# Kernel optimization log

Measured on AMD Instinct MI355X. Metric: run time of the kernel, lower is better.

## Reference

```python
import jax, jax.numpy as jnp
import numpy as np

B, C, H, W = 8, 512, 48, 48
DK = C // 8            # query/key dim
L = max(H, W)          # rel_pos_length == H == W
R = 2 * L - 1          # num relative shifts
N = H * W
EPS = 1e-5


def setup_inputs() -> dict:
    key = jax.random.key(0)
    ks = jax.random.split(key, 20)
    d = {
        "x": jax.random.normal(ks[0], (B, C, H, W), jnp.float32),
        "Wq": jax.random.normal(ks[1], (DK, C), jnp.float32) * 0.02,
        "bq": jnp.zeros((DK,), jnp.float32),
        "q_scale": jnp.ones((DK,), jnp.float32),
        "q_bias": jnp.zeros((DK,), jnp.float32),
        "Wk": jax.random.normal(ks[2], (DK, C), jnp.float32) * 0.02,
        "bk": jnp.zeros((DK,), jnp.float32),
        "k_scale": jnp.ones((DK,), jnp.float32),
        "k_bias": jnp.zeros((DK,), jnp.float32),
        "Wv": jax.random.normal(ks[3], (C, C), jnp.float32) * 0.02,
        "bv": jnp.zeros((C,), jnp.float32),
        "v_scale": jnp.ones((C,), jnp.float32),
        "v_bias": jnp.zeros((C,), jnp.float32),
        "rel_rows": jax.random.normal(ks[4], (R, DK), jnp.float32),
        "rel_columns": jax.random.normal(ks[5], (R, DK), jnp.float32),
        "bnr_scale": jnp.ones((C,), jnp.float32),
        "bnr_bias": jnp.zeros((C,), jnp.float32),
        "bnc_scale": jnp.ones((C,), jnp.float32),
        "bnc_bias": jnp.zeros((C,), jnp.float32),
        # gamma is a learned scalar (init 0 in torch; nonzero here so output != x)
        "gamma": jax.random.normal(ks[6], (1,), jnp.float32) * 0.1,
    }
    return d


def _bn(y, scale, bias):
    # train-mode BatchNorm2d: batch stats over (B,H,W), biased variance
    m = jnp.mean(y, axis=(0, 2, 3))
    v = jnp.mean((y - m[None, :, None, None]) ** 2, axis=(0, 2, 3))
    yn = (y - m[None, :, None, None]) * jax.lax.rsqrt(v + EPS)[None, :, None, None]
    return yn * scale[None, :, None, None] + bias[None, :, None, None]


def _conv_bn_relu(x, Wc, bc, scale, bias):
    y = jnp.einsum('bchw,oc->bohw', x, Wc) + bc[None, :, None, None]  # 1x1 conv
    return jax.nn.relu(_bn(y, scale, bias))


def _rel_P(l, rel_table):
    # compute_reindexing_tensor reduces to a one-hot over shift (i - x) since
    # |i-x| <= L always holds when L == l; Ih @ rel_table == gather by shift.
    x = jnp.arange(l)[:, None]
    i = jnp.arange(l)[None, :]
    idx = i - x + (L - 1)                 # (l, l) in [0, 2L-2]
    return rel_table[idx]                 # (l, l, DK)


def reference(x, Wq, bq, q_scale, q_bias, Wk, bk, k_scale, k_bias,
              Wv, bv, v_scale, v_bias, rel_rows, rel_columns,
              bnr_scale, bnr_bias, bnc_scale, bnc_bias, gamma):
    q = _conv_bn_relu(x, Wq, bq, q_scale, q_bias).reshape(B, DK, N)   # proj_query^T
    k = _conv_bn_relu(x, Wk, bk, k_scale, k_bias).reshape(B, DK, N)
    v = _conv_bn_relu(x, Wv, bv, v_scale, v_bias).reshape(B, C, N)

    energy = jnp.einsum('bdn,bdm->bnm', q, k)        # (B,N,N) = Q^T K (unscaled)
    attention = jax.nn.softmax(energy, axis=-1)
    out = jnp.einsum('bcj,bij->bci', v, attention)   # V A^T
    attn_mask = out.reshape(B, C, H, W)

    # relative position terms: Eh = V (Ph Q^T), Ew = V (Pw Q^T)
    Ph = _rel_P(H, rel_rows).reshape(N, DK)          # (N,DK) since H==W
    Mh = jnp.einsum('nd,bdm->bnm', Ph, q)
    Eh = jnp.einsum('bcn,bnm->bcm', v, Mh).reshape(B, C, H, W)
    Eh = _bn(Eh, bnr_scale, bnr_bias)

    Pw = _rel_P(W, rel_columns).reshape(N, DK)
    Mw = jnp.einsum('nd,bdm->bnm', Pw, q)
    Ew = jnp.einsum('bcn,bnm->bcm', v, Mw).reshape(B, C, H, W)
    Ew = _bn(Ew, bnc_scale, bnc_bias)

    attn_mask = attn_mask + Eh + Ew
    return gamma[0] * attn_mask + x
```

## Files before the change

### kernel.cpp

```cpp
#include <hip/hip_runtime.h>
#include <math.h>

#define BB   8
#define CIN  512
#define NSP  2304
#define OCH  640
#define LL   48

typedef __attribute__((ext_vector_type(8))) short bf16x8;
typedef __attribute__((ext_vector_type(8))) unsigned short u16x8;
typedef __attribute__((ext_vector_type(4))) float f32x4;

__device__ inline unsigned short f2bf(float f) {
  unsigned int u = __float_as_uint(f);
  unsigned int r = (u + 0x7fffu + ((u >> 16) & 1u)) >> 16;
  return (unsigned short)r;
}
__device__ inline float bf2f(unsigned short h) {
  return __uint_as_float(((unsigned int)h) << 16);
}


#define STAGE128x64(GP, LD, LDSN)                                              \
  {                                                                            \
    const unsigned short* gsrc_ = (GP);                                        \
    _Pragma("unroll") for (int cc_ = 0; cc_ < 4; cc_++) {                      \
      int base_ = w * 2048 + cc_ * 512;                                        \
      int row_ = w * 32 + cc_ * 8 + rsub;                                      \
      __builtin_amdgcn_global_load_lds(                                        \
          (const __attribute__((address_space(1))) void*)(gsrc_ +              \
              (size_t)row_ * (LD) + scolb),                                    \
          (__attribute__((address_space(3))) void*)&(LDSN)[base_], 16, 0, 0);  \
    }                                                                          \
  }

#define STAGE8(GPA, LDA, LA, GPB, LDB, LB)                                     \
  {                                                                            \
    if (w < 4) {                                                               \
      const unsigned short* gsrc_ = (GPA);                                     \
      _Pragma("unroll") for (int cc_ = 0; cc_ < 4; cc_++) {                    \
        int base_ = w * 2048 + cc_ * 512;                                      \
        int row_ = w * 32 + cc_ * 8 + rsub;                                    \
        __builtin_amdgcn_global_load_lds(                                      \
            (const __attribute__((address_space(1))) void*)(gsrc_ +            \
                (size_t)row_ * (LDA) + scolb),                                 \
            (__attribute__((address_space(3))) void*)&(LA)[base_], 16, 0, 0);  \
      }                                                                        \
    } else {                                                                   \
      const unsigned short* gsrc_ = (GPB);                                     \
      int w2_ = w - 4;                                                         \
      _Pragma("unroll") for (int cc_ = 0; cc_ < 4; cc_++) {                    \
        int base_ = w2_ * 2048 + cc_ * 512;                                    \
        int row_ = w2_ * 32 + cc_ * 8 + rsub;                                  \
        __builtin_amdgcn_global_load_lds(                                      \
            (const __attribute__((address_space(1))) void*)(gsrc_ +            \
                (size_t)row_ * (LDB) + scolb),                                 \
            (__attribute__((address_space(3))) void*)&(LB)[base_], 16, 0, 0);  \
      }                                                                        \
    }                                                                          \
  }

#define MFMA_STEP(APTR, BPTR)                                                  \
  _Pragma("unroll") for (int kk_ = 0; kk_ < 2; kk_++) {                        \
    bf16x8 af_[4], bf_[4];                                                     \
    int kcol_ = (((kk_ * 4 + (lane >> 4)) ^ (lane & 7)) * 8);                  \
    _Pragma("unroll") for (int m_ = 0; m_ < 4; m_++)                           \
      af_[m_] = *(const bf16x8*)&(APTR)[(wr * 64 + m_ * 16 + (lane & 15)) * 64 + kcol_]; \
    _Pragma("unroll") for (int n_ = 0; n_ < 4; n_++)                           \
      bf_[n_] = *(const bf16x8*)&(BPTR)[(wc * 64 + n_ * 16 + (lane & 15)) * 64 + kcol_]; \
    _Pragma("unroll") for (int m_ = 0; m_ < 4; m_++)                           \
      _Pragma("unroll") for (int n_ = 0; n_ < 4; n_++)                         \
        acc[m_][n_] = __builtin_amdgcn_mfma_f32_16x16x32_bf16(                 \
            af_[m_], bf_[n_], acc[m_][n_], 0, 0, 0);                           \
  }

#define MFMA_STEP8(APTR, BPTR)                                                 \
  _Pragma("unroll") for (int kk_ = 0; kk_ < 2; kk_++) {                        \
    bf16x8 af_[4], bf_[2];                                                     \
    int kcol_ = (((kk_ * 4 + (lane >> 4)) ^ (lane & 7)) * 8);                  \
    _Pragma("unroll") for (int m_ = 0; m_ < 4; m_++)                           \
      af_[m_] = *(const bf16x8*)&(APTR)[(wr * 64 + m_ * 16 + (lane & 15)) * 64 + kcol_]; \
    _Pragma("unroll") for (int n_ = 0; n_ < 2; n_++)                           \
      bf_[n_] = *(const bf16x8*)&(BPTR)[(wc * 32 + n_ * 16 + (lane & 15)) * 64 + kcol_]; \
    _Pragma("unroll") for (int m_ = 0; m_ < 4; m_++)                           \
      _Pragma("unroll") for (int n_ = 0; n_ < 2; n_++)                         \
        acc[m_][n_] = __builtin_amdgcn_mfma_f32_16x16x32_bf16(                 \
            af_[m_], bf_[n_], acc[m_][n_], 0, 0, 0);                           \
  }

#define MFMA_PROLOG()                                                          \
  const int tid = threadIdx.x;                                                 \
  const int lane = tid & 63;                                                   \
  const int w = tid >> 6;                                                      \
  const int wr = w >> 1, wc = w & 1;                                           \
  const int rsub = lane >> 3;                                                  \
  const int scolb = ((lane & 7) ^ rsub) * 8;                                   \
  f32x4 acc[4][4] = {};                                                        \
  (void)scolb; (void)rsub; (void)wr; (void)wc;

__global__ __launch_bounds__(256) void prep_all(
    const float* __restrict__ Wq, const float* __restrict__ bq,
    const float* __restrict__ Wk, const float* __restrict__ bk,
    const float* __restrict__ Wv, const float* __restrict__ bv,
    const float* __restrict__ rel_rows, const float* __restrict__ rel_cols,
    unsigned short* __restrict__ Wstb, float* __restrict__ bst,
    unsigned short* __restrict__ Pcatb) {
  int idx = blockIdx.x * 256 + threadIdx.x;
  if (idx < OCH * CIN) {
    int row = idx >> 9;
    float val;
    if (row < 64)       val = Wq[idx];
    else if (row < 128) val = Wk[idx - (64 << 9)];
    else                val = Wv[idx - (128 << 9)];
    Wstb[idx] = f2bf(val);
    if (idx < OCH) {
      float bval;
      if (idx < 64)       bval = bq[idx];
      else if (idx < 128) bval = bk[idx - 64];
      else                bval = bv[idx - 128];
      bst[idx] = bval;
    }
  } else {
    int p = idx - OCH * CIN;
    int dd = p / NSP;
    int n = p - dd * NSP;
    int xr = n / LL;
    int ic = n - xr * LL;
    int shift = ic - xr + (LL - 1);
    float val = (dd < 64) ? rel_rows[shift * 64 + dd]
                          : rel_cols[shift * 64 + (dd - 64)];
    Pcatb[p] = f2bf(val);
  }
}

__global__ __launch_bounds__(256) void transpose_x(
    const float* __restrict__ x, unsigned short* __restrict__ xTb) {
  __shared__ float t[64][65];
  const int n0 = blockIdx.x * 64;
  const int c0 = blockIdx.y * 64;
  const int b = blockIdx.z;
  const int j = threadIdx.x & 63;
  const int g = threadIdx.x >> 6;
  const float* xp = x + (size_t)b * CIN * NSP;
#pragma unroll
  for (int i = 0; i < 16; i++) {
    int cl = g * 16 + i;
    t[cl][j] = xp[(size_t)(c0 + cl) * NSP + n0 + j];
  }
  __syncthreads();
  unsigned short* op = xTb + (size_t)b * NSP * CIN;
#pragma unroll
  for (int i = 0; i < 16; i++) {
    int nl = g * 16 + i;
    op[(size_t)(n0 + nl) * CIN + c0 + j] = f2bf(t[j][nl]);
  }
}

__global__ __launch_bounds__(256) void proj_mfma(
    const unsigned short* __restrict__ Wstb, const float* __restrict__ bst,
    const unsigned short* __restrict__ xTb, unsigned short* __restrict__ y16,
    float* __restrict__ part1, float* __restrict__ part2) {
  __shared__ unsigned short As[2][8192];
  __shared__ unsigned short Bs[2][8192];
  int sw = ((blockIdx.x & 7) * 90) + (blockIdx.x >> 3);
  const int rb = sw % 5;
  const int nb = (sw / 5) % 18;
  const int b = sw / 90;
  const int r0 = rb * 128;
  const int n0 = nb * 128;
  MFMA_PROLOG();
  const unsigned short* A = Wstb + (size_t)r0 * CIN;
  const unsigned short* B = xTb + (size_t)b * NSP * CIN + (size_t)n0 * CIN;

  STAGE128x64(A, CIN, As[0]);
  STAGE128x64(B, CIN, Bs[0]);
  asm volatile("s_waitcnt vmcnt(0)" ::: "memory");
  __builtin_amdgcn_sched_barrier(0);
  __builtin_amdgcn_s_barrier();

  int cur = 0;
  for (int t = 0; t < 8; ++t) {
    if (t + 1 < 8) {
      STAGE128x64(A + (t + 1) * 64, CIN, As[cur ^ 1]);
      STAGE128x64(B + (t + 1) * 64, CIN, Bs[cur ^ 1]);
    }
    __builtin_amdgcn_s_setprio(1);
    MFMA_STEP(As[cur], Bs[cur]);
    __builtin_amdgcn_s_setprio(0);
    asm volatile("s_waitcnt vmcnt(0)" ::: "memory");
    __builtin_amdgcn_sched_barrier(0);
    __builtin_amdgcn_s_barrier();
    cur ^= 1;
  }

  float* sp = (float*)&As[0][0];
#pragma unroll
  for (int m = 0; m < 4; m++) {
#pragma unroll
    for (int r = 0; r < 4; r++) {
      int rl = wr * 64 + m * 16 + (lane >> 4) * 4 + r;
      int row = r0 + rl;
      float bias = bst[row];
      float s1 = 0.f, s2 = 0.f;
#pragma unroll
      for (int n = 0; n < 4; n++) {
        float yv = acc[m][n][r] + bias;
        s1 += yv;
        s2 += yv * yv;
        y16[((size_t)b * OCH + row) * NSP + n0 + wc * 64 + n * 16 + (lane & 15)] = f2bf(yv);
      }
#pragma unroll
      for (int off = 1; off < 16; off <<= 1) {
        s1 += __shfl_xor(s1, off);
        s2 += __shfl_xor(s2, off);
      }
      if ((lane & 15) == 0) {
        sp[rl * 2 + wc] = s1;
        sp[256 + rl * 2 + wc] = s2;
      }
    }
  }
  __syncthreads();
  if (tid < 128) {
    size_t pbase = ((size_t)b * 18 + nb) * OCH + r0 + tid;
    part1[pbase] = sp[tid * 2] + sp[tid * 2 + 1];
    part2[pbase] = sp[256 + tid * 2] + sp[256 + tid * 2 + 1];
  }
}

__global__ __launch_bounds__(256) void bn_finalize(
    const float* __restrict__ part1, const float* __restrict__ part2,
    const float* __restrict__ qs_, const float* __restrict__ qb_,
    const float* __restrict__ ks_, const float* __restrict__ kb_,
    const float* __restrict__ vs_, const float* __restrict__ vb_,
    float* __restrict__ chanA, float* __restrict__ chanB) {
  const int ch = blockIdx.x;
  const int tid = threadIdx.x;
  float s1 = 0.f, s2 = 0.f;
  for (int t = tid; t < 144; t += 256) {
    s1 += part1[(size_t)t * OCH + ch];
    s2 += part2[(size_t)t * OCH + ch];
  }
  __shared__ float sb[8];
#pragma unroll
  for (int off = 32; off > 0; off >>= 1) {
    s1 += __shfl_down(s1, off);
    s2 += __shfl_down(s2, off);
  }
  int lane = tid & 63, wid = tid >> 6;
  if (lane == 0) { sb[wid] = s1; sb[4 + wid] = s2; }
  __syncthreads();
  if (tid == 0) {
    float ts  = sb[0] + sb[1] + sb[2] + sb[3];
    float ts2 = sb[4] + sb[5] + sb[6] + sb[7];
    const float inv = 1.f / (float)(BB * NSP);
    float mean = ts * inv;
    float var  = ts2 * inv - mean * mean;
    float scale, bias;
    if (ch < 64)       { scale = qs_[ch];       bias = qb_[ch]; }
    else if (ch < 128) { scale = ks_[ch - 64];  bias = kb_[ch - 64]; }
    else               { scale = vs_[ch - 128]; bias = vb_[ch - 128]; }
    float a = scale * rsqrtf(var + 1e-5f);
    chanA[ch] = a;
    chanB[ch] = bias - mean * a;
  }
}

__global__ __launch_bounds__(256) void bn_post(
    unsigned short* __restrict__ y16, const float* __restrict__ chanA,
    const float* __restrict__ chanB, unsigned short* __restrict__ qTb,
    unsigned short* __restrict__ kTb) {
  __shared__ unsigned short qk[128][64];
  const int n0 = blockIdx.x * 64;
  const int b = blockIdx.y;
  const int tid = threadIdx.x;
#pragma unroll
  for (int k = 0; k < 20; k++) {
    int v = tid + k * 256;
    int ch = v >> 3;
    int n8 = (v & 7) * 8;
    size_t off = ((size_t)b * OCH + ch) * NSP + n0 + n8;
    float a = chanA[ch], bo = chanB[ch];
    ushort4 u0 = *(ushort4*)&y16[off];
    ushort4 u1 = *(ushort4*)&y16[off + 4];
    ushort4 o0, o1;
    o0.x = f2bf(fmaxf(0.f, a * bf2f(u0.x) + bo));
    o0.y = f2bf(fmaxf(0.f, a * bf2f(u0.y) + bo));
    o0.z = f2bf(fmaxf(0.f, a * bf2f(u0.z) + bo));
    o0.w = f2bf(fmaxf(0.f, a * bf2f(u0.w) + bo));
    o1.x = f2bf(fmaxf(0.f, a * bf2f(u1.x) + bo));
    o1.y = f2bf(fmaxf(0.f, a * bf2f(u1.y) + bo));
    o1.z = f2bf(fmaxf(0.f, a * bf2f(u1.z) + bo));
    o1.w = f2bf(fmaxf(0.f, a * bf2f(u1.w) + bo));
    *(ushort4*)&y16[off] = o0;
    *(ushort4*)&y16[off + 4] = o1;
    if (ch < 128) {
      *(ushort4*)&qk[ch][n8] = o0;
      *(ushort4*)&qk[ch][n8 + 4] = o1;
    }
  }
  __syncthreads();
#pragma unroll
  for (int it = 0; it < 4; it++) {
    int combo = (tid >> 6) + it * 4;
    int plane = combo >> 3;
    int dg = combo & 7;
    int nl = tid & 63;
    unsigned short tmp[8];
#pragma unroll
    for (int d = 0; d < 8; d++) tmp[d] = qk[plane * 64 + dg * 8 + d][nl];
    unsigned short* out = (plane == 0) ? qTb : kTb;
    *(u16x8*)&out[((size_t)b * NSP + n0 + nl) * 64 + dg * 8] = *(u16x8*)tmp;
  }
}

__global__ __launch_bounds__(256) void qsum_kernel(
    const unsigned short* __restrict__ y16, float* __restrict__ qs) {
  int bd = blockIdx.x;
  int b = bd >> 6, d = bd & 63;
  const ushort4* p = (const ushort4*)(y16 + ((size_t)b * OCH + d) * NSP);
  float s = 0.f;
  for (int t = threadIdx.x; t < NSP / 4; t += 256) {
    ushort4 u = p[t];
    s += bf2f(u.x) + bf2f(u.y) + bf2f(u.z) + bf2f(u.w);
  }
  __shared__ float sb[4];
#pragma unroll
  for (int off = 32; off > 0; off >>= 1) s += __shfl_down(s, off);
  int lane = threadIdx.x & 63, wid = threadIdx.x >> 6;
  if (lane == 0) sb[wid] = s;
  __syncthreads();
  if (threadIdx.x == 0) qs[bd] = sb[0] + sb[1] + sb[2] + sb[3];
}

__global__ __launch_bounds__(256) void gq_mfma(
    const unsigned short* __restrict__ y16, float* __restrict__ Gqp) {
  __shared__ float wlds[4 * 4096];
  const int bx = blockIdx.x;
  const int b = bx >> 2, kc = bx & 3;
  const int tid = threadIdx.x;
  const int lane = tid & 63;
  const int w = tid >> 6;
  const unsigned short* q = y16 + (size_t)b * OCH * NSP;
  f32x4 acc[4][4] = {};
  for (int k0 = kc * 576 + w * 32; k0 < (kc + 1) * 576; k0 += 128) {
    bf16x8 fr[4];
#pragma unroll
    for (int f = 0; f < 4; f++) {
      int row = f * 16 + (lane & 15);
      fr[f] = *(const bf16x8*)&q[(size_t)row * NSP + k0 + (lane >> 4) * 8];
    }
#pragma unroll
    for (int fm = 0; fm < 4; fm++)
#pragma unroll
      for (int fn = 0; fn < 4; fn++)
        acc[fm][fn] = __builtin_amdgcn_mfma_f32_16x16x32_bf16(
            fr[fm], fr[fn], acc[fm][fn], 0, 0, 0);
  }
#pragma unroll
  for (int fm = 0; fm < 4; fm++)
#pragma unroll
    for (int fn = 0; fn < 4; fn++)
#pragma unroll
      for (int r = 0; r < 4; r++) {
        int d = fm * 16 + (lane >> 4) * 4 + r;
        int e = fn * 16 + (lane & 15);
        wlds[w * 4096 + d * 64 + e] = acc[fm][fn][r];
      }
  __syncthreads();
  for (int t = tid; t < 4096; t += 256)
    Gqp[(size_t)bx * 4096 + t] =
        wlds[t] + wlds[4096 + t] + wlds[8192 + t] + wlds[12288 + t];
}

__global__ __launch_bounds__(256) void energy_mfma(
    const unsigned short* __restrict__ qTb, const unsigned short* __restrict__ kTb,
    unsigned short* __restrict__ Pp, float* __restrict__ Ppart) {
  __shared__ unsigned short As[8192];
  __shared__ unsigned short Bs[8192];
  int sw = ((blockIdx.x & 7) * 324) + (blockIdx.x >> 3);
  const int jb = sw % 18;
  const int ib = (sw / 18) % 18;
  const int b = sw / 324;
  const int i0 = ib * 128;
  const int j0 = jb * 128;
  MFMA_PROLOG();
  STAGE128x64(qTb + ((size_t)b * NSP + i0) * 64, 64, As);
  STAGE128x64(kTb + ((size_t)b * NSP + j0) * 64, 64, Bs);
  __syncthreads();
  MFMA_STEP(As, Bs);
  __syncthreads();
  float* sp = (float*)As;
  unsigned short* pp = Pp + (size_t)b * NSP * NSP;
#pragma unroll
  for (int m = 0; m < 4; m++) {
#pragma unroll
    for (int r = 0; r < 4; r++) {
      int rl = wr * 64 + m * 16 + (lane >> 4) * 4 + r;
      int i = i0 + rl;
      float s1 = 0.f;
#pragma unroll
      for (int n = 0; n < 4; n++) {
        int j = j0 + wc * 64 + n * 16 + (lane & 15);
        unsigned short h = f2bf(__expf(acc[m][n][r]));
        pp[(size_t)i * NSP + j] = h;
        s1 += bf2f(h);
      }
#pragma unroll
      for (int off = 1; off < 16; off <<= 1) s1 += __shfl_xor(s1, off);
      if ((lane & 15) == 0) sp[rl * 2 + wc] = s1;
    }
  }
  __syncthreads();
  if (tid < 128)
    Ppart[((size_t)b * 18 + jb) * NSP + i0 + tid] = sp[tid * 2] + sp[tid * 2 + 1];
}

__global__ __launch_bounds__(256) void up_mfma(
    const unsigned short* __restrict__ y16, const unsigned short* __restrict__ Pcatb,
    float* __restrict__ Upart) {
  __shared__ unsigned short As[2][8192];
  __shared__ unsigned short Bs[2][8192];
  int sw = ((blockIdx.x & 7) * 24) + (blockIdx.x >> 3);
  const int cb = sw % 4;
  const int kc = (sw / 4) % 6;
  const int b = sw / 24;
  const int c0 = cb * 128;
  MFMA_PROLOG();
  const unsigned short* A = y16 + ((size_t)b * OCH + 128 + c0) * NSP + kc * 384;
  const unsigned short* B = Pcatb + kc * 384;

  STAGE128x64(A, NSP, As[0]);
  STAGE128x64(B, NSP, Bs[0]);
  asm volatile("s_waitcnt vmcnt(0)" ::: "memory");
  __builtin_amdgcn_sched_barrier(0);
  __builtin_amdgcn_s_barrier();

  int cur = 0;
  for (int t = 0; t < 6; ++t) {
    if (t + 1 < 6) {
      STAGE128x64(A + (t + 1) * 64, NSP, As[cur ^ 1]);
      STAGE128x64(B + (t + 1) * 64, NSP, Bs[cur ^ 1]);
    }
    __builtin_amdgcn_s_setprio(1);
    MFMA_STEP(As[cur], Bs[cur]);
    __builtin_amdgcn_s_setprio(0);
    asm volatile("s_waitcnt vmcnt(0)" ::: "memory");
    __builtin_amdgcn_sched_barrier(0);
    __builtin_amdgcn_s_barrier();
    cur ^= 1;
  }

  float* up = Upart + ((size_t)kc * BB + b) * CIN * 128 + (size_t)c0 * 128;
#pragma unroll
  for (int m = 0; m < 4; m++)
#pragma unroll
    for (int r = 0; r < 4; r++) {
      int rl = wr * 64 + m * 16 + (lane >> 4) * 4 + r;
#pragma unroll
      for (int n = 0; n < 4; n++) {
        int col = wc * 64 + n * 16 + (lane & 15);
        up[(size_t)rl * 128 + col] = acc[m][n][r];
      }
    }
}

__global__ __launch_bounds__(256) void rel_finalize(
    const float* __restrict__ Upart, const float* __restrict__ Gqp,
    const float* __restrict__ qs,
    const float* __restrict__ bnr_s, const float* __restrict__ bnr_b,
    const float* __restrict__ bnc_s, const float* __restrict__ bnc_b,
    float* __restrict__ offc, unsigned short* __restrict__ Ucb) {
  const int c = blockIdx.x;
  const int tid = threadIdx.x;
  __shared__ float U[8][128];
  __shared__ float ghw[2];
  for (int t = tid; t < 1024; t += 256) {
    int b = t >> 7, dd = t & 127;
    float s = 0.f;
#pragma unroll
    for (int kc = 0; kc < 6; kc++)
      s += Upart[(((size_t)kc * BB + b) * CIN + c) * 128 + dd];
    U[b][dd] = s;
  }
  __syncthreads();
  if (tid < 64) {
    const int d = tid;
    float s1h = 0.f, s2h = 0.f, s1w = 0.f, s2w = 0.f;
    for (int b = 0; b < BB; b++) {
      float uh = U[b][d], uw = U[b][64 + d];
      float th = 0.f, tw = 0.f;
#pragma unroll
      for (int kc = 0; kc < 4; kc++) {
        const float* G = Gqp + ((size_t)(b * 4 + kc)) * 4096 + d * 64;
        for (int e = 0; e < 64; e++) {
          float g = G[e];
          th += g * U[b][e];
          tw += g * U[b][64 + e];
        }
      }
      float qsd = qs[b * 64 + d];
      s1h += uh * qsd;
      s2h += uh * th;
      s1w += uw * qsd;
      s2w += uw * tw;
    }
#pragma unroll
    for (int off = 32; off > 0; off >>= 1) {
      s1h += __shfl_down(s1h, off);
      s2h += __shfl_down(s2h, off);
      s1w += __shfl_down(s1w, off);
      s2w += __shfl_down(s2w, off);
    }
    if (d == 0) {
      const float inv = 1.f / (float)(BB * NSP);
      float mh = s1h * inv, vh = s2h * inv - mh * mh;
      float mw = s1w * inv, vw = s2w * inv - mw * mw;
      float gch = bnr_s[c] * rsqrtf(vh + 1e-5f);
      float gcw = bnc_s[c] * rsqrtf(vw + 1e-5f);
      ghw[0] = gch;
      ghw[1] = gcw;
      offc[c] = (bnr_b[c] - mh * gch) + (bnc_b[c] - mw * gcw);
    }
  }
  __syncthreads();
  for (int t = tid; t < 512; t += 256) {
    int b = t >> 6, d = t & 63;
    Ucb[((size_t)b * CIN + c) * 64 + d] =
        f2bf(U[b][d] * ghw[0] + U[b][64 + d] * ghw[1]);
  }
}

__global__ __launch_bounds__(512) void attn_fused_gemm(
    const unsigned short* __restrict__ y16,
    const unsigned short* __restrict__ Pp,
    const float* __restrict__ Ppart,
    const unsigned short* __restrict__ Ucb,
    const unsigned short* __restrict__ qTb,
    const float* __restrict__ offc,
    const float* __restrict__ gammap,
    const float* __restrict__ x,
    float* __restrict__ dst) {
  __shared__ unsigned short As[2][8192];
  __shared__ unsigned short Bs[2][8192];
  __shared__ float rzl[128];
  int sw = ((blockIdx.x & 7) * 72) + (blockIdx.x >> 3);
  const int cb = sw % 4;
  const int ib = (sw / 4) % 18;
  const int b = sw / 72;
  const int c0 = cb * 128;
  const int i0 = ib * 128;
  const int tid = threadIdx.x;
  const int lane = tid & 63;
  const int w = tid >> 6;
  const int wr = w >> 2, wc = w & 3;
  const int rsub = lane >> 3;
  const int scolb = ((lane & 7) ^ rsub) * 8;
  f32x4 acc[4][2] = {};

  const unsigned short* A = y16 + ((size_t)b * OCH + 128 + c0) * NSP;
  const unsigned short* B = Pp + (size_t)b * NSP * NSP + (size_t)i0 * NSP;
  const unsigned short* A2 = Ucb + (size_t)b * CIN * 64 + (size_t)c0 * 64;
  const unsigned short* B2 = qTb + (size_t)b * NSP * 64 + (size_t)i0 * 64;

  STAGE8(A, NSP, As[0], B, NSP, Bs[0]);
  if (tid < 128) {
    float s = 0.f;
#pragma unroll
    for (int jb = 0; jb < 18; jb++)
      s += Ppart[((size_t)b * 18 + jb) * NSP + i0 + tid];
    rzl[tid] = 1.f / s;
  }
  asm volatile("s_waitcnt vmcnt(0)" ::: "memory");
  __builtin_amdgcn_sched_barrier(0);
  __builtin_amdgcn_s_barrier();

  int cur = 0;
  for (int tt = 0; tt < 37; ++tt) {
    if (tt + 1 < 36) {
      STAGE8(A + (tt + 1) * 64, NSP, As[cur ^ 1], B + (tt + 1) * 64, NSP, Bs[cur ^ 1]);
    } else if (tt + 1 == 36) {
      STAGE8(A2, 64, As[cur ^ 1], B2, 64, Bs[cur ^ 1]);
    }
    if (tt == 36) {
#pragma unroll
      for (int n = 0; n < 2; n++) {
        float rz = rzl[wc * 32 + n * 16 + (lane & 15)];
#pragma unroll
        for (int m = 0; m < 4; m++)
#pragma unroll
          for (int r = 0; r < 4; r++) acc[m][n][r] *= rz;
      }
    }
    __builtin_amdgcn_s_setprio(1);
    MFMA_STEP8(As[cur], Bs[cur]);
    __builtin_amdgcn_s_setprio(0);
    asm volatile("s_waitcnt vmcnt(0)" ::: "memory");
    __builtin_amdgcn_sched_barrier(0);
    __builtin_amdgcn_s_barrier();
    cur ^= 1;
  }

  const float gmm = gammap[0];
  const float* xp = x + (size_t)b * CIN * NSP;
  float* dp = dst + (size_t)b * CIN * NSP;
#pragma unroll
  for (int m = 0; m < 4; m++) {
#pragma unroll
    for (int r = 0; r < 4; r++) {
      int c = c0 + wr * 64 + m * 16 + (lane >> 4) * 4 + r;
      float off = offc[c];
#pragma unroll
      for (int n = 0; n < 2; n++) {
        int i = i0 + wc * 32 + n * 16 + (lane & 15);
        size_t o = (size_t)c * NSP + i;
        dp[o] = gmm * (acc[m][n][r] + off) + xp[o];
      }
    }
  }
}

extern "C" void kernel_launch(void* const* d_in, const int* in_sizes, int n_in,
                              void* d_out, int out_size, void* d_ws, size_t ws_size,
                              hipStream_t stream) {
  const float* x        = (const float*)d_in[0];
  const float* Wq       = (const float*)d_in[1];
  const float* bq       = (const float*)d_in[2];
  const float* q_scale  = (const float*)d_in[3];
  const float* q_bias   = (const float*)d_in[4];
  const float* Wk       = (const float*)d_in[5];
  const float* bk       = (const float*)d_in[6];
  const float* k_scale  = (const float*)d_in[7];
  const float* k_bias   = (const float*)d_in[8];
  const float* Wv       = (const float*)d_in[9];
  const float* bv       = (const float*)d_in[10];
  const float* v_scale  = (const float*)d_in[11];
  const float* v_bias   = (const float*)d_in[12];
  const float* rel_rows = (const float*)d_in[13];
  const float* rel_cols = (const float*)d_in[14];
  const float* bnr_s    = (const float*)d_in[15];
  const float* bnr_b    = (const float*)d_in[16];
  const float* bnc_s    = (const float*)d_in[17];
  const float* bnc_b    = (const float*)d_in[18];
  const float* gamma    = (const float*)d_in[19];
  float* dst = (float*)d_out;

  float* ws = (float*)d_ws;
  size_t o = 0;
  unsigned short* Wstb = (unsigned short*)(ws + o); o += (size_t)OCH * CIN / 2;
  float* bst    = ws + o; o += 1024;
  float* chanA  = ws + o; o += 1024;
  float* chanB  = ws + o; o += 1024;
  unsigned short* Pcatb = (unsigned short*)(ws + o); o += (size_t)128 * NSP / 2;
  unsigned short* y16 = (unsigned short*)(ws + o); o += (size_t)BB * OCH * NSP / 2;
  unsigned short* xTb = (unsigned short*)(ws + o); o += (size_t)BB * NSP * CIN / 2;
  unsigned short* Pp  = (unsigned short*)(ws + o); o += (size_t)BB * NSP * NSP / 2;
  float* Ppart  = ws + o; o += (size_t)BB * 18 * NSP;
  float* Upart  = ws + o; o += (size_t)6 * BB * CIN * 128;
  float* Gqp    = ws + o; o += (size_t)32 * 4096;
  float* part1  = ws + o; o += (size_t)BB * 18 * OCH;
  float* part2  = ws + o; o += (size_t)BB * 18 * OCH;
  float* qs     = ws + o; o += 1024;
  float* offc   = ws + o; o += 1024;
  unsigned short* qTb = (unsigned short*)(ws + o); o += (size_t)BB * NSP * 64 / 2;
  unsigned short* kTb = (unsigned short*)(ws + o); o += (size_t)BB * NSP * 64 / 2;
  unsigned short* Ucb = (unsigned short*)(ws + o); o += (size_t)BB * CIN * 64 / 2;

  prep_all<<<(OCH * CIN + 128 * NSP) / 256, 256, 0, stream>>>(
      Wq, bq, Wk, bk, Wv, bv, rel_rows, rel_cols, Wstb, bst, Pcatb);
  transpose_x<<<dim3(NSP / 64, CIN / 64, BB), 256, 0, stream>>>(x, xTb);

  proj_mfma<<<720, 256, 0, stream>>>(Wstb, bst, xTb, y16, part1, part2);
  bn_finalize<<<OCH, 256, 0, stream>>>(part1, part2, q_scale, q_bias, k_scale,
                                       k_bias, v_scale, v_bias, chanA, chanB);
  bn_post<<<dim3(36, BB), 256, 0, stream>>>(y16, chanA, chanB, qTb, kTb);
  qsum_kernel<<<BB * 64, 256, 0, stream>>>(y16, qs);
  gq_mfma<<<32, 256, 0, stream>>>(y16, Gqp);

  energy_mfma<<<2592, 256, 0, stream>>>(qTb, kTb, Pp, Ppart);

  up_mfma<<<192, 256, 0, stream>>>(y16, Pcatb, Upart);
  rel_finalize<<<CIN, 256, 0, stream>>>(Upart, Gqp, qs, bnr_s, bnr_b,
                                        bnc_s, bnc_b, offc, Ucb);

  attn_fused_gemm<<<576, 512, 0, stream>>>(y16, Pp, Ppart, Ucb, qTb, offc, gamma, x, dst);
}
```

Baseline: 240.2 us.

## Fuse energy/exp computation into attention GEMM as flash-style kernel

Removes the separate energy kernel that wrote the full bf16 exp(QK^T) matrix and row-sum partials to global memory. A new fused kernel computes QK^T tiles on the fly, exponentiates them, accumulates row sums, and immediately multiplies by V. Each block now covers all 512 channels for 32 query positions, so exp(QK) is recomputed per block instead of being read back. This avoids the large P matrix round trip at the cost of V loaded directly from global memory without LDS staging and smaller per-block tiles.

```diff
diff --git a/kernel.cpp b/kernel.cpp
--- a/kernel.cpp
+++ b/kernel.cpp
@@ -6,6 +6,9 @@
 #define NSP  2304
 #define OCH  640
 #define LL   48
+
+#define AS1 __attribute__((address_space(1)))
+#define AS3 __attribute__((address_space(3)))
 
 typedef __attribute__((ext_vector_type(8))) short bf16x8;
 typedef __attribute__((ext_vector_type(8))) unsigned short u16x8;
@@ -28,35 +31,8 @@
       int base_ = w * 2048 + cc_ * 512;                                        \
       int row_ = w * 32 + cc_ * 8 + rsub;                                      \
       __builtin_amdgcn_global_load_lds(                                        \
-          (const __attribute__((address_space(1))) void*)(gsrc_ +              \
-              (size_t)row_ * (LD) + scolb),                                    \
-          (__attribute__((address_space(3))) void*)&(LDSN)[base_], 16, 0, 0);  \
-    }                                                                          \
-  }
-
-#define STAGE8(GPA, LDA, LA, GPB, LDB, LB)                                     \
-  {                                                                            \
-    if (w < 4) {                                                               \
-      const unsigned short* gsrc_ = (GPA);                                     \
-      _Pragma("unroll") for (int cc_ = 0; cc_ < 4; cc_++) {                    \
-        int base_ = w * 2048 + cc_ * 512;                                      \
-        int row_ = w * 32 + cc_ * 8 + rsub;                                    \
-        __builtin_amdgcn_global_load_lds(                                      \
-            (const __attribute__((address_space(1))) void*)(gsrc_ +            \
-                (size_t)row_ * (LDA) + scolb),                                 \
-            (__attribute__((address_space(3))) void*)&(LA)[base_], 16, 0, 0);  \
-      }                                                                        \
-    } else {                                                                   \
-      const unsigned short* gsrc_ = (GPB);                                     \
-      int w2_ = w - 4;                                                         \
-      _Pragma("unroll") for (int cc_ = 0; cc_ < 4; cc_++) {                    \
-        int base_ = w2_ * 2048 + cc_ * 512;                                    \
-        int row_ = w2_ * 32 + cc_ * 8 + rsub;                                  \
-        __builtin_amdgcn_global_load_lds(                                      \
-            (const __attribute__((address_space(1))) void*)(gsrc_ +            \
-                (size_t)row_ * (LDB) + scolb),                                 \
-            (__attribute__((address_space(3))) void*)&(LB)[base_], 16, 0, 0);  \
-      }                                                                        \
+          (const AS1 void*)(gsrc_ + (size_t)row_ * (LD) + scolb),              \
+          (AS3 void*)&(LDSN)[base_], 16, 0, 0);                                \
     }                                                                          \
   }
 
@@ -70,20 +46,6 @@
       bf_[n_] = *(const bf16x8*)&(BPTR)[(wc * 64 + n_ * 16 + (lane & 15)) * 64 + kcol_]; \
     _Pragma("unroll") for (int m_ = 0; m_ < 4; m_++)                           \
       _Pragma("unroll") for (int n_ = 0; n_ < 4; n_++)                         \
-        acc[m_][n_] = __builtin_amdgcn_mfma_f32_16x16x32_bf16(                 \
-            af_[m_], bf_[n_], acc[m_][n_], 0, 0, 0);                           \
-  }
-
-#define MFMA_STEP8(APTR, BPTR)                                                 \
-  _Pragma("unroll") for (int kk_ = 0; kk_ < 2; kk_++) {                        \
-    bf16x8 af_[4], bf_[2];                                                     \
-    int kcol_ = (((kk_ * 4 + (lane >> 4)) ^ (lane & 7)) * 8);                  \
-    _Pragma("unroll") for (int m_ = 0; m_ < 4; m_++)                           \
-      af_[m_] = *(const bf16x8*)&(APTR)[(wr * 64 + m_ * 16 + (lane & 15)) * 64 + kcol_]; \
-    _Pragma("unroll") for (int n_ = 0; n_ < 2; n_++)                           \
-      bf_[n_] = *(const bf16x8*)&(BPTR)[(wc * 32 + n_ * 16 + (lane & 15)) * 64 + kcol_]; \
-    _Pragma("unroll") for (int m_ = 0; m_ < 4; m_++)                           \
-      _Pragma("unroll") for (int n_ = 0; n_ < 2; n_++)                         \
         acc[m_][n_] = __builtin_amdgcn_mfma_f32_16x16x32_bf16(                 \
             af_[m_], bf_[n_], acc[m_][n_], 0, 0, 0);                           \
   }
@@ -373,49 +335,6 @@
         wlds[t] + wlds[4096 + t] + wlds[8192 + t] + wlds[12288 + t];
 }
 
-__global__ __launch_bounds__(256) void energy_mfma(
-    const unsigned short* __restrict__ qTb, const unsigned short* __restrict__ kTb,
-    unsigned short* __restrict__ Pp, float* __restrict__ Ppart) {
-  __shared__ unsigned short As[8192];
-  __shared__ unsigned short Bs[8192];
-  int sw = ((blockIdx.x & 7) * 324) + (blockIdx.x >> 3);
-  const int jb = sw % 18;
-  const int ib = (sw / 18) % 18;
-  const int b = sw / 324;
-  const int i0 = ib * 128;
-  const int j0 = jb * 128;
-  MFMA_PROLOG();
-  STAGE128x64(qTb + ((size_t)b * NSP + i0) * 64, 64, As);
-  STAGE128x64(kTb + ((size_t)b * NSP + j0) * 64, 64, Bs);
-  __syncthreads();
-  MFMA_STEP(As, Bs);
-  __syncthreads();
-  float* sp = (float*)As;
-  unsigned short* pp = Pp + (size_t)b * NSP * NSP;
-#pragma unroll
-  for (int m = 0; m < 4; m++) {
-#pragma unroll
-    for (int r = 0; r < 4; r++) {
-      int rl = wr * 64 + m * 16 + (lane >> 4) * 4 + r;
-      int i = i0 + rl;
-      float s1 = 0.f;
-#pragma unroll
-      for (int n = 0; n < 4; n++) {
-        int j = j0 + wc * 64 + n * 16 + (lane & 15);
-        unsigned short h = f2bf(__expf(acc[m][n][r]));
-        pp[(size_t)i * NSP + j] = h;
-        s1 += bf2f(h);
-      }
-#pragma unroll
-      for (int off = 1; off < 16; off <<= 1) s1 += __shfl_xor(s1, off);
-      if ((lane & 15) == 0) sp[rl * 2 + wc] = s1;
-    }
-  }
-  __syncthreads();
-  if (tid < 128)
-    Ppart[((size_t)b * 18 + jb) * NSP + i0 + tid] = sp[tid * 2] + sp[tid * 2 + 1];
-}
-
 __global__ __launch_bounds__(256) void up_mfma(
     const unsigned short* __restrict__ y16, const unsigned short* __restrict__ Pcatb,
     float* __restrict__ Upart) {
@@ -531,74 +450,164 @@
   }
 }
 
-__global__ __launch_bounds__(512) void attn_fused_gemm(
+__global__ __launch_bounds__(512) void flash_attn(
     const unsigned short* __restrict__ y16,
-    const unsigned short* __restrict__ Pp,
-    const float* __restrict__ Ppart,
+    const unsigned short* __restrict__ qTb,
+    const unsigned short* __restrict__ kTb,
     const unsigned short* __restrict__ Ucb,
-    const unsigned short* __restrict__ qTb,
     const float* __restrict__ offc,
     const float* __restrict__ gammap,
     const float* __restrict__ x,
     float* __restrict__ dst) {
-  __shared__ unsigned short As[2][8192];
-  __shared__ unsigned short Bs[2][8192];
-  __shared__ float rzl[128];
+  __shared__ unsigned short q_lds[32 * 64];
+  __shared__ unsigned short k_lds[2][64 * 64];
+  __shared__ unsigned short p_lds[2][32 * 64];
+  __shared__ float rsum[4][32];
+  __shared__ float rzl[32];
   int sw = ((blockIdx.x & 7) * 72) + (blockIdx.x >> 3);
-  const int cb = sw % 4;
-  const int ib = (sw / 4) % 18;
+  const int ib = sw % 72;
   const int b = sw / 72;
-  const int c0 = cb * 128;
-  const int i0 = ib * 128;
+  const int i0 = ib * 32;
   const int tid = threadIdx.x;
   const int lane = tid & 63;
   const int w = tid >> 6;
-  const int wr = w >> 2, wc = w & 3;
   const int rsub = lane >> 3;
-  const int scolb = ((lane & 7) ^ rsub) * 8;
+  const int scol = ((lane & 7) ^ rsub) * 8;
+  const int l15 = lane & 15;
+  const int l4 = lane >> 4;
+  const int iSub = w & 1, jSub = w >> 1;
   f32x4 acc[4][2] = {};
-
-  const unsigned short* A = y16 + ((size_t)b * OCH + 128 + c0) * NSP;
-  const unsigned short* B = Pp + (size_t)b * NSP * NSP + (size_t)i0 * NSP;
-  const unsigned short* A2 = Ucb + (size_t)b * CIN * 64 + (size_t)c0 * 64;
-  const unsigned short* B2 = qTb + (size_t)b * NSP * 64 + (size_t)i0 * 64;
-
-  STAGE8(A, NSP, As[0], B, NSP, Bs[0]);
-  if (tid < 128) {
-    float s = 0.f;
-#pragma unroll
-    for (int jb = 0; jb < 18; jb++)
-      s += Ppart[((size_t)b * 18 + jb) * NSP + i0 + tid];
-    rzl[tid] = 1.f / s;
+  float rs0 = 0.f, rs1 = 0.f, rs2 = 0.f, rs3 = 0.f;
+
+  const unsigned short* qsrc = qTb + ((size_t)b * NSP + i0) * 64;
+  const unsigned short* ksrc = kTb + (size_t)b * NSP * 64;
+  const unsigned short* vsrc = y16 + ((size_t)b * OCH + 128) * NSP;
+
+  if (w < 4) {
+    __builtin_amdgcn_global_load_lds(
+        (const AS1 void*)(qsrc + (size_t)(w * 8 + rsub) * 64 + scol),
+        (AS3 void*)&q_lds[w * 512], 16, 0, 0);
+  } else {
+    int w4 = w - 4;
+    __builtin_amdgcn_global_load_lds(
+        (const AS1 void*)(ksrc + (size_t)(w4 * 16 + rsub) * 64 + scol),
+        (AS3 void*)&k_lds[0][w4 * 1024], 16, 0, 0);
+    __builtin_amdgcn_global_load_lds(
+        (const AS1 void*)(ksrc + (size_t)(w4 * 16 + 8 + rsub) * 64 + scol),
+        (AS3 void*)&k_lds[0][w4 * 1024 + 512], 16, 0, 0);
   }
   asm volatile("s_waitcnt vmcnt(0)" ::: "memory");
   __builtin_amdgcn_sched_barrier(0);
   __builtin_amdgcn_s_barrier();
 
   int cur = 0;
-  for (int tt = 0; tt < 37; ++tt) {
-    if (tt + 1 < 36) {
-      STAGE8(A + (tt + 1) * 64, NSP, As[cur ^ 1], B + (tt + 1) * 64, NSP, Bs[cur ^ 1]);
-    } else if (tt + 1 == 36) {
-      STAGE8(A2, 64, As[cur ^ 1], B2, 64, Bs[cur ^ 1]);
-    }
-    if (tt == 36) {
-#pragma unroll
-      for (int n = 0; n < 2; n++) {
-        float rz = rzl[wc * 32 + n * 16 + (lane & 15)];
-#pragma unroll
-        for (int m = 0; m < 4; m++)
-#pragma unroll
-          for (int r = 0; r < 4; r++) acc[m][n][r] *= rz;
-      }
-    }
-    __builtin_amdgcn_s_setprio(1);
-    MFMA_STEP8(As[cur], Bs[cur]);
-    __builtin_amdgcn_s_setprio(0);
-    asm volatile("s_waitcnt vmcnt(0)" ::: "memory");
+  for (int t = 0; t < 36; ++t) {
+    if (t + 1 < 36) {
+      __builtin_amdgcn_global_load_lds(
+          (const AS1 void*)(ksrc + (size_t)((t + 1) * 64 + w * 8 + rsub) * 64 + scol),
+          (AS3 void*)&k_lds[cur ^ 1][w * 512], 16, 0, 0);
+    }
+    bf16x8 av[4][2];
+#pragma unroll
+    for (int m = 0; m < 4; m++)
+#pragma unroll
+      for (int kk = 0; kk < 2; kk++)
+        av[m][kk] = *(const bf16x8*)&vsrc[(size_t)(w * 64 + m * 16 + l15) * NSP
+                                          + t * 64 + kk * 32 + l4 * 8];
+    f32x4 e = {};
+#pragma unroll
+    for (int kk = 0; kk < 2; kk++) {
+      int kcol = ((kk * 4 + l4) ^ (lane & 7)) * 8;
+      bf16x8 aq = *(const bf16x8*)&q_lds[(iSub * 16 + l15) * 64 + kcol];
+      bf16x8 bk = *(const bf16x8*)&k_lds[cur][(jSub * 16 + l15) * 64 + kcol];
+      e = __builtin_amdgcn_mfma_f32_16x16x32_bf16(aq, bk, e, 0, 0, 0);
+    }
+    float p0 = __expf(e[0]), p1 = __expf(e[1]);
+    float p2 = __expf(e[2]), p3 = __expf(e[3]);
+    float q0 = p0, q1 = p1, q2 = p2, q3 = p3;
+#pragma unroll
+    for (int off = 1; off < 16; off <<= 1) {
+      q0 += __shfl_xor(q0, off);
+      q1 += __shfl_xor(q1, off);
+      q2 += __shfl_xor(q2, off);
+      q3 += __shfl_xor(q3, off);
+    }
+    rs0 += q0; rs1 += q1; rs2 += q2; rs3 += q3;
+    {
+      int j = jSub * 16 + l15;
+      int jslot = j >> 3, jel = j & 7;
+      unsigned short* pl = p_lds[cur];
+      float pv[4] = {p0, p1, p2, p3};
+#pragma unroll
+      for (int r = 0; r < 4; r++) {
+        int i = iSub * 16 + l4 * 4 + r;
+        pl[i * 64 + ((jslot ^ (i & 7)) * 8 + jel)] = f2bf(pv[r]);
+      }
+    }
+    asm volatile("s_waitcnt vmcnt(0) lgkmcnt(0)" ::: "memory");
     __builtin_amdgcn_sched_barrier(0);
     __builtin_amdgcn_s_barrier();
+    __builtin_amdgcn_s_setprio(1);
+#pragma unroll
+    for (int kk = 0; kk < 2; kk++) {
+      bf16x8 bp[2];
+#pragma unroll
+      for (int n = 0; n < 2; n++) {
+        int row = n * 16 + l15;
+        int kcol = ((kk * 4 + l4) ^ (row & 7)) * 8;
+        bp[n] = *(const bf16x8*)&p_lds[cur][row * 64 + kcol];
+      }
+#pragma unroll
+      for (int m = 0; m < 4; m++)
+#pragma unroll
+        for (int n = 0; n < 2; n++)
+          acc[m][n] = __builtin_amdgcn_mfma_f32_16x16x32_bf16(
+              av[m][kk], bp[n], acc[m][n], 0, 0, 0);
+    }
+    __builtin_amdgcn_s_setprio(0);
     cur ^= 1;
+  }
+
+  if (l15 == 0) {
+    int ibase = iSub * 16 + l4 * 4;
+    rsum[jSub][ibase + 0] = rs0;
+    rsum[jSub][ibase + 1] = rs1;
+    rsum[jSub][ibase + 2] = rs2;
+    rsum[jSub][ibase + 3] = rs3;
+  }
+  __syncthreads();
+  if (tid < 32)
+    rzl[tid] = 1.f / (rsum[0][tid] + rsum[1][tid] + rsum[2][tid] + rsum[3][tid]);
+  __syncthreads();
+
+#pragma unroll
+  for (int n = 0; n < 2; n++) {
+    float rz = rzl[n * 16 + l15];
+#pragma unroll
+    for (int m = 0; m < 4; m++)
+#pragma unroll
+      for (int r = 0; r < 4; r++) acc[m][n][r] *= rz;
+  }
+
+  const unsigned short* A2 = Ucb + (size_t)b * CIN * 64;
+#pragma unroll
+  for (int kk = 0; kk < 2; kk++) {
+    bf16x8 bq[2];
+#pragma unroll
+    for (int n = 0; n < 2; n++) {
+      int row = n * 16 + l15;
+      int kcol = ((kk * 4 + l4) ^ (row & 7)) * 8;
+      bq[n] = *(const bf16x8*)&q_lds[row * 64 + kcol];
+    }
+#pragma unroll
+    for (int m = 0; m < 4; m++) {
+      bf16x8 au = *(const bf16x8*)&A2[(size_t)(w * 64 + m * 16 + l15) * 64
+                                      + kk * 32 + l4 * 8];
+#pragma unroll
+      for (int n = 0; n < 2; n++)
+        acc[m][n] = __builtin_amdgcn_mfma_f32_16x16x32_bf16(
+            au, bq[n], acc[m][n], 0, 0, 0);
+    }
   }
 
   const float gmm = gammap[0];
@@ -608,11 +617,11 @@
   for (int m = 0; m < 4; m++) {
 #pragma unroll
     for (int r = 0; r < 4; r++) {
-      int c = c0 + wr * 64 + m * 16 + (lane >> 4) * 4 + r;
+      int c = w * 64 + m * 16 + l4 * 4 + r;
       float off = offc[c];
 #pragma unroll
       for (int n = 0; n < 2; n++) {
-        int i = i0 + wc * 32 + n * 16 + (lane & 15);
+        int i = i0 + n * 16 + l15;
         size_t o = (size_t)c * NSP + i;
         dp[o] = gmm * (acc[m][n][r] + off) + xp[o];
       }
@@ -654,8 +663,6 @@
   unsigned short* Pcatb = (unsigned short*)(ws + o); o += (size_t)128 * NSP / 2;
   unsigned short* y16 = (unsigned short*)(ws + o); o += (size_t)BB * OCH * NSP / 2;
   unsigned short* xTb = (unsigned short*)(ws + o); o += (size_t)BB * NSP * CIN / 2;
-  unsigned short* Pp  = (unsigned short*)(ws + o); o += (size_t)BB * NSP * NSP / 2;
-  float* Ppart  = ws + o; o += (size_t)BB * 18 * NSP;
   float* Upart  = ws + o; o += (size_t)6 * BB * CIN * 128;
   float* Gqp    = ws + o; o += (size_t)32 * 4096;
   float* part1  = ws + o; o += (size_t)BB * 18 * OCH;
@@ -677,11 +684,9 @@
   qsum_kernel<<<BB * 64, 256, 0, stream>>>(y16, qs);
   gq_mfma<<<32, 256, 0, stream>>>(y16, Gqp);
 
-  energy_mfma<<<2592, 256, 0, stream>>>(qTb, kTb, Pp, Ppart);
-
   up_mfma<<<192, 256, 0, stream>>>(y16, Pcatb, Upart);
   rel_finalize<<<CIN, 256, 0, stream>>>(Upart, Gqp, qs, bnr_s, bnr_b,
                                         bnc_s, bnc_b, offc, Ucb);
 
-  attn_fused_gemm<<<576, 512, 0, stream>>>(y16, Pp, Ppart, Ucb, qTb, offc, gamma, x, dst);
-}
+  flash_attn<<<576, 512, 0, stream>>>(y16, qTb, kTb, Ucb, offc, gamma, x, dst);
+}
```

New measurement: 376.6 us. 56.8% more time.

## Coalesce energy P stores via LDS and load attention B operand directly to registers

Applied to the files above, without the earlier changes.

In energy_mfma, the exp'd bf16 probabilities are first written to shared memory and then written to global memory as 16-byte vectors, so the scattered 2-byte stores become coalesced row stores. In attn_fused_gemm, the P (B operand) tiles are no longer staged through LDS. Each wave loads its fragments straight from global into registers with double buffering and partial vmcnt waits, and only A goes through LDS. The rank-64 relative-position GEMM tail is moved out of the pipelined loop into a separate direct-from-global MFMA step after the softmax rescale. This frees LDS and removes the B staging traffic, at the cost of more register pressure and uncoalesced per-lane global reads of P.

```diff
diff --git a/kernel.cpp b/kernel.cpp
--- a/kernel.cpp
+++ b/kernel.cpp
@@ -6,6 +6,9 @@
 #define NSP  2304
 #define OCH  640
 #define LL   48
+
+#define AS1 __attribute__((address_space(1)))
+#define AS3 __attribute__((address_space(3)))
 
 typedef __attribute__((ext_vector_type(8))) short bf16x8;
 typedef __attribute__((ext_vector_type(8))) unsigned short u16x8;
@@ -28,35 +31,8 @@
       int base_ = w * 2048 + cc_ * 512;                                        \
       int row_ = w * 32 + cc_ * 8 + rsub;                                      \
       __builtin_amdgcn_global_load_lds(                                        \
-          (const __attribute__((address_space(1))) void*)(gsrc_ +              \
-              (size_t)row_ * (LD) + scolb),                                    \
-          (__attribute__((address_space(3))) void*)&(LDSN)[base_], 16, 0, 0);  \
-    }                                                                          \
-  }
-
-#define STAGE8(GPA, LDA, LA, GPB, LDB, LB)                                     \
-  {                                                                            \
-    if (w < 4) {                                                               \
-      const unsigned short* gsrc_ = (GPA);                                     \
-      _Pragma("unroll") for (int cc_ = 0; cc_ < 4; cc_++) {                    \
-        int base_ = w * 2048 + cc_ * 512;                                      \
-        int row_ = w * 32 + cc_ * 8 + rsub;                                    \
-        __builtin_amdgcn_global_load_lds(                                      \
-            (const __attribute__((address_space(1))) void*)(gsrc_ +            \
-                (size_t)row_ * (LDA) + scolb),                                 \
-            (__attribute__((address_space(3))) void*)&(LA)[base_], 16, 0, 0);  \
-      }                                                                        \
-    } else {                                                                   \
-      const unsigned short* gsrc_ = (GPB);                                     \
-      int w2_ = w - 4;                                                         \
-      _Pragma("unroll") for (int cc_ = 0; cc_ < 4; cc_++) {                    \
-        int base_ = w2_ * 2048 + cc_ * 512;                                    \
-        int row_ = w2_ * 32 + cc_ * 8 + rsub;                                  \
-        __builtin_amdgcn_global_load_lds(                                      \
-            (const __attribute__((address_space(1))) void*)(gsrc_ +            \
-                (size_t)row_ * (LDB) + scolb),                                 \
-            (__attribute__((address_space(3))) void*)&(LB)[base_], 16, 0, 0);  \
-      }                                                                        \
+          (const AS1 void*)(gsrc_ + (size_t)row_ * (LD) + scolb),              \
+          (AS3 void*)&(LDSN)[base_], 16, 0, 0);                                \
     }                                                                          \
   }
 
@@ -70,20 +46,6 @@
       bf_[n_] = *(const bf16x8*)&(BPTR)[(wc * 64 + n_ * 16 + (lane & 15)) * 64 + kcol_]; \
     _Pragma("unroll") for (int m_ = 0; m_ < 4; m_++)                           \
       _Pragma("unroll") for (int n_ = 0; n_ < 4; n_++)                         \
-        acc[m_][n_] = __builtin_amdgcn_mfma_f32_16x16x32_bf16(                 \
-            af_[m_], bf_[n_], acc[m_][n_], 0, 0, 0);                           \
-  }
-
-#define MFMA_STEP8(APTR, BPTR)                                                 \
-  _Pragma("unroll") for (int kk_ = 0; kk_ < 2; kk_++) {                        \
-    bf16x8 af_[4], bf_[2];                                                     \
-    int kcol_ = (((kk_ * 4 + (lane >> 4)) ^ (lane & 7)) * 8);                  \
-    _Pragma("unroll") for (int m_ = 0; m_ < 4; m_++)                           \
-      af_[m_] = *(const bf16x8*)&(APTR)[(wr * 64 + m_ * 16 + (lane & 15)) * 64 + kcol_]; \
-    _Pragma("unroll") for (int n_ = 0; n_ < 2; n_++)                           \
-      bf_[n_] = *(const bf16x8*)&(BPTR)[(wc * 32 + n_ * 16 + (lane & 15)) * 64 + kcol_]; \
-    _Pragma("unroll") for (int m_ = 0; m_ < 4; m_++)                           \
-      _Pragma("unroll") for (int n_ = 0; n_ < 2; n_++)                         \
         acc[m_][n_] = __builtin_amdgcn_mfma_f32_16x16x32_bf16(                 \
             af_[m_], bf_[n_], acc[m_][n_], 0, 0, 0);                           \
   }
@@ -376,8 +338,8 @@
 __global__ __launch_bounds__(256) void energy_mfma(
     const unsigned short* __restrict__ qTb, const unsigned short* __restrict__ kTb,
     unsigned short* __restrict__ Pp, float* __restrict__ Ppart) {
-  __shared__ unsigned short As[8192];
-  __shared__ unsigned short Bs[8192];
+  __shared__ unsigned short lds[16384];
+  __shared__ float rs[256];
   int sw = ((blockIdx.x & 7) * 324) + (blockIdx.x >> 3);
   const int jb = sw % 18;
   const int ib = (sw / 18) % 18;
@@ -385,35 +347,39 @@
   const int i0 = ib * 128;
   const int j0 = jb * 128;
   MFMA_PROLOG();
-  STAGE128x64(qTb + ((size_t)b * NSP + i0) * 64, 64, As);
-  STAGE128x64(kTb + ((size_t)b * NSP + j0) * 64, 64, Bs);
-  __syncthreads();
-  MFMA_STEP(As, Bs);
-  __syncthreads();
-  float* sp = (float*)As;
-  unsigned short* pp = Pp + (size_t)b * NSP * NSP;
+  STAGE128x64(qTb + ((size_t)b * NSP + i0) * 64, 64, lds);
+  STAGE128x64(kTb + ((size_t)b * NSP + j0) * 64, 64, (lds + 8192));
+  __syncthreads();
+  MFMA_STEP(lds, (lds + 8192));
+  __syncthreads();
 #pragma unroll
   for (int m = 0; m < 4; m++) {
 #pragma unroll
     for (int r = 0; r < 4; r++) {
       int rl = wr * 64 + m * 16 + (lane >> 4) * 4 + r;
-      int i = i0 + rl;
       float s1 = 0.f;
 #pragma unroll
       for (int n = 0; n < 4; n++) {
-        int j = j0 + wc * 64 + n * 16 + (lane & 15);
         unsigned short h = f2bf(__expf(acc[m][n][r]));
-        pp[(size_t)i * NSP + j] = h;
+        lds[rl * 128 + wc * 64 + n * 16 + (lane & 15)] = h;
         s1 += bf2f(h);
       }
 #pragma unroll
       for (int off = 1; off < 16; off <<= 1) s1 += __shfl_xor(s1, off);
-      if ((lane & 15) == 0) sp[rl * 2 + wc] = s1;
-    }
-  }
-  __syncthreads();
+      if ((lane & 15) == 0) rs[rl * 2 + wc] = s1;
+    }
+  }
+  __syncthreads();
+  unsigned short* pp = Pp + (size_t)b * NSP * NSP;
+#pragma unroll
+  for (int c8 = tid; c8 < 2048; c8 += 256) {
+    int il = c8 >> 4;
+    int jl = (c8 & 15) * 8;
+    u16x8 v = *(const u16x8*)&lds[il * 128 + jl];
+    *(u16x8*)&pp[(size_t)(i0 + il) * NSP + j0 + jl] = v;
+  }
   if (tid < 128)
-    Ppart[((size_t)b * 18 + jb) * NSP + i0 + tid] = sp[tid * 2] + sp[tid * 2 + 1];
+    Ppart[((size_t)b * 18 + jb) * NSP + i0 + tid] = rs[tid * 2] + rs[tid * 2 + 1];
 }
 
 __global__ __launch_bounds__(256) void up_mfma(
@@ -542,7 +508,6 @@
     const float* __restrict__ x,
     float* __restrict__ dst) {
   __shared__ unsigned short As[2][8192];
-  __shared__ unsigned short Bs[2][8192];
   __shared__ float rzl[128];
   int sw = ((blockIdx.x & 7) * 72) + (blockIdx.x >> 3);
   const int cb = sw % 4;
@@ -556,14 +521,46 @@
   const int wr = w >> 2, wc = w & 3;
   const int rsub = lane >> 3;
   const int scolb = ((lane & 7) ^ rsub) * 8;
+  const int l15 = lane & 15, l4 = lane >> 4;
   f32x4 acc[4][2] = {};
 
   const unsigned short* A = y16 + ((size_t)b * OCH + 128 + c0) * NSP;
-  const unsigned short* B = Pp + (size_t)b * NSP * NSP + (size_t)i0 * NSP;
-  const unsigned short* A2 = Ucb + (size_t)b * CIN * 64 + (size_t)c0 * 64;
-  const unsigned short* B2 = qTb + (size_t)b * NSP * 64 + (size_t)i0 * 64;
-
-  STAGE8(A, NSP, As[0], B, NSP, Bs[0]);
+  const unsigned short* Bp = Pp + (size_t)b * NSP * NSP + (size_t)i0 * NSP;
+
+#define STAGEA(GP, LDSN)                                                       \
+  {                                                                            \
+    _Pragma("unroll") for (int cc_ = 0; cc_ < 2; cc_++) {                      \
+      int row_ = w * 16 + cc_ * 8 + rsub;                                      \
+      __builtin_amdgcn_global_load_lds(                                        \
+          (const AS1 void*)((GP) + (size_t)row_ * NSP + scolb),                \
+          (AS3 void*)&(LDSN)[w * 1024 + cc_ * 512], 16, 0, 0);                 \
+    }                                                                          \
+  }
+
+#define LOADB(BF, SRC, LD, KOFF)                                               \
+  {                                                                            \
+    _Pragma("unroll") for (int n_ = 0; n_ < 2; n_++)                           \
+      _Pragma("unroll") for (int kk_ = 0; kk_ < 2; kk_++)                      \
+        BF[n_][kk_] = *(const bf16x8*)&(SRC)[(size_t)(wc * 32 + n_ * 16 + l15) * (LD) \
+                                             + (KOFF) + kk_ * 32 + l4 * 8];    \
+  }
+
+#define MFMAREG(LDSN, BF)                                                      \
+  _Pragma("unroll") for (int kk_ = 0; kk_ < 2; kk_++) {                        \
+    bf16x8 af_[4];                                                             \
+    int kcol_ = (((kk_ * 4 + l4) ^ (lane & 7)) * 8);                           \
+    _Pragma("unroll") for (int m_ = 0; m_ < 4; m_++)                           \
+      af_[m_] = *(const bf16x8*)&(LDSN)[(wr * 64 + m_ * 16 + l15) * 64 + kcol_]; \
+    _Pragma("unroll") for (int m_ = 0; m_ < 4; m_++)                           \
+      _Pragma("unroll") for (int n_ = 0; n_ < 2; n_++)                         \
+        acc[m_][n_] = __builtin_amdgcn_mfma_f32_16x16x32_bf16(                 \
+            af_[m_], BF[n_][kk_], acc[m_][n_], 0, 0, 0);                       \
+  }
+
+  bf16x8 bf0[2][2], bf1[2][2];
+
+  STAGEA(A, As[0]);
+  LOADB(bf0, Bp, NSP, 0);
   if (tid < 128) {
     float s = 0.f;
 #pragma unroll
@@ -571,34 +568,61 @@
       s += Ppart[((size_t)b * 18 + jb) * NSP + i0 + tid];
     rzl[tid] = 1.f / s;
   }
-  asm volatile("s_waitcnt vmcnt(0)" ::: "memory");
+  asm volatile("s_waitcnt vmcnt(4)" ::: "memory");
   __builtin_amdgcn_sched_barrier(0);
   __builtin_amdgcn_s_barrier();
 
-  int cur = 0;
-  for (int tt = 0; tt < 37; ++tt) {
-    if (tt + 1 < 36) {
-      STAGE8(A + (tt + 1) * 64, NSP, As[cur ^ 1], B + (tt + 1) * 64, NSP, Bs[cur ^ 1]);
-    } else if (tt + 1 == 36) {
-      STAGE8(A2, 64, As[cur ^ 1], B2, 64, Bs[cur ^ 1]);
-    }
-    if (tt == 36) {
-#pragma unroll
-      for (int n = 0; n < 2; n++) {
-        float rz = rzl[wc * 32 + n * 16 + (lane & 15)];
-#pragma unroll
-        for (int m = 0; m < 4; m++)
-#pragma unroll
-          for (int r = 0; r < 4; r++) acc[m][n][r] *= rz;
-      }
-    }
+  for (int t = 0; t < 36; t += 2) {
+    STAGEA(A + (t + 1) * 64, As[1]);
+    LOADB(bf1, Bp, NSP, (t + 1) * 64);
     __builtin_amdgcn_s_setprio(1);
-    MFMA_STEP8(As[cur], Bs[cur]);
+    MFMAREG(As[0], bf0);
     __builtin_amdgcn_s_setprio(0);
-    asm volatile("s_waitcnt vmcnt(0)" ::: "memory");
+    asm volatile("s_waitcnt vmcnt(4)" ::: "memory");
     __builtin_amdgcn_sched_barrier(0);
     __builtin_amdgcn_s_barrier();
-    cur ^= 1;
+    if (t + 2 < 36) {
+      STAGEA(A + (t + 2) * 64, As[0]);
+      LOADB(bf0, Bp, NSP, (t + 2) * 64);
+    }
+    __builtin_amdgcn_s_setprio(1);
+    MFMAREG(As[1], bf1);
+    __builtin_amdgcn_s_setprio(0);
+    if (t + 2 < 36) {
+      asm volatile("s_waitcnt vmcnt(4)" ::: "memory");
+    } else {
+      asm volatile("s_waitcnt vmcnt(0)" ::: "memory");
+    }
+    __builtin_amdgcn_sched_barrier(0);
+    __builtin_amdgcn_s_barrier();
+  }
+
+#pragma unroll
+  for (int n = 0; n < 2; n++) {
+    float rz = rzl[wc * 32 + n * 16 + l15];
+#pragma unroll
+    for (int m = 0; m < 4; m++)
+#pragma unroll
+      for (int r = 0; r < 4; r++) acc[m][n][r] *= rz;
+  }
+
+  {
+    const unsigned short* A2 = Ucb + (size_t)b * CIN * 64;
+    const unsigned short* B2 = qTb + ((size_t)b * NSP + i0) * 64;
+    bf16x8 bfr[2][2];
+    LOADB(bfr, B2, 64, 0);
+#pragma unroll
+    for (int kk = 0; kk < 2; kk++) {
+#pragma unroll
+      for (int m = 0; m < 4; m++) {
+        bf16x8 au = *(const bf16x8*)&A2[(size_t)(c0 + wr * 64 + m * 16 + l15) * 64
+                                        + kk * 32 + l4 * 8];
+#pragma unroll
+        for (int n = 0; n < 2; n++)
+          acc[m][n] = __builtin_amdgcn_mfma_f32_16x16x32_bf16(
+              au, bfr[n][kk], acc[m][n], 0, 0, 0);
+      }
+    }
   }
 
   const float gmm = gammap[0];
@@ -608,16 +632,19 @@
   for (int m = 0; m < 4; m++) {
 #pragma unroll
     for (int r = 0; r < 4; r++) {
-      int c = c0 + wr * 64 + m * 16 + (lane >> 4) * 4 + r;
+      int c = c0 + wr * 64 + m * 16 + l4 * 4 + r;
       float off = offc[c];
 #pragma unroll
       for (int n = 0; n < 2; n++) {
-        int i = i0 + wc * 32 + n * 16 + (lane & 15);
+        int i = i0 + wc * 32 + n * 16 + l15;
         size_t o = (size_t)c * NSP + i;
         dp[o] = gmm * (acc[m][n][r] + off) + xp[o];
       }
     }
   }
+#undef STAGEA
+#undef LOADB
+#undef MFMAREG
 }
 
 extern "C" void kernel_launch(void* const* d_in, const int* in_sizes, int n_in,
@@ -683,5 +710,6 @@
   rel_finalize<<<CIN, 256, 0, stream>>>(Upart, Gqp, qs, bnr_s, bnr_b,
                                         bnc_s, bnc_b, offc, Ucb);
 
-  attn_fused_gemm<<<576, 512, 0, stream>>>(y16, Pp, Ppart, Ucb, qTb, offc, gamma, x, dst);
-}
+  attn_fused_gemm<<<576, 512, 0, stream>>>(y16, Pp, Ppart, Ucb, qTb, offc,
+                                           gamma, x, dst);
+}
```

Result: slower. 305.0 us (+27.0%).
